# Performance work log

Measured on AMD Instinct MI355X. Metric: run time of the kernel, lower is better.

Reference implementation:

```python
import jax, jax.numpy as jnp
import numpy as np

E = 768
H = 8

def setup_inputs() -> dict:
    key = jax.random.key(0)
    ks = jax.random.split(key, 9)
    s = 1.0 / np.sqrt(E)
    x = jax.random.normal(ks[0], (4, 2048, E), dtype=jnp.float32)
    Wq = jax.random.uniform(ks[1], (E, E), jnp.float32, -s, s)
    bq = jax.random.uniform(ks[2], (E,), jnp.float32, -s, s)
    Wk = jax.random.uniform(ks[3], (E, E), jnp.float32, -s, s)
    bk = jax.random.uniform(ks[4], (E,), jnp.float32, -s, s)
    Wv = jax.random.uniform(ks[5], (E, E), jnp.float32, -s, s)
    bv = jax.random.uniform(ks[6], (E,), jnp.float32, -s, s)
    Wo = jax.random.uniform(ks[7], (E, E), jnp.float32, -s, s)
    bo = jax.random.uniform(ks[8], (E,), jnp.float32, -s, s)
    return {"x": x, "Wq": Wq, "bq": bq, "Wk": Wk, "bk": bk, "Wv": Wv, "bv": bv, "Wo": Wo, "bo": bo}

def reference(x, Wq, bq, Wk, bk, Wv, bv, Wo, bo):
    B, N, Emb = x.shape
    d = Emb // H
    # projections (torch Linear: y = x @ W.T + b)
    q = (x @ Wq.T + bq).reshape(B, N, H, d).transpose(0, 2, 1, 3)  # [B,H,N,d]
    k = (x @ Wk.T + bk).reshape(B, N, H, d).transpose(0, 2, 1, 3)
    v = (x @ Wv.T + bv).reshape(B, N, H, d).transpose(0, 2, 1, 3)
    scores = jnp.einsum('bhnd,bhmd->bhnm', q, k) / jnp.sqrt(jnp.float32(d))
    attn = jax.nn.softmax(scores, axis=-1)  # dropout p=0.0 -> identity
    out = jnp.einsum('bhnm,bhmd->bhnd', attn, v)
    out = out.transpose(0, 2, 1, 3).reshape(B, N, Emb)
    return out @ Wo.T + bo
```

## Files before the change

### kernel.cpp

```cpp
#include <hip/hip_runtime.h>


#define E_DIM 768
#define N_HEAD 8
#define D_HEAD 96
#define B_SZ 4
#define N_SEQ 2048
#define BN (B_SZ * N_SEQ)

typedef unsigned short u16;
typedef __attribute__((ext_vector_type(8))) unsigned short u16x8;
typedef __attribute__((ext_vector_type(4))) unsigned short u16x4;
typedef __attribute__((ext_vector_type(8))) short s16x8;
typedef __attribute__((ext_vector_type(4))) float f32x4;

#define SZ_X   ((size_t)BN * E_DIM)
#define SZ_W   ((size_t)E_DIM * E_DIM)
#define SZ_B   ((size_t)E_DIM)
#define N_CONV (SZ_X + 4 * SZ_W + 4 * SZ_B)

__device__ __forceinline__ float bf2f(u16 u) {
    union { unsigned u; float f; } c; c.u = ((unsigned)u) << 16; return c.f;
}
__device__ __forceinline__ u16 f2bf(float f) {
    union { float f; unsigned u; } c; c.f = f;
    unsigned r = c.u + 0x7FFFu + ((c.u >> 16) & 1u);
    return (u16)(r >> 16);
}
__device__ __forceinline__ void gl_lds16(const u16* g, u16* l) {
    __builtin_amdgcn_global_load_lds(
        (const __attribute__((address_space(1))) unsigned int*)g,
        (__attribute__((address_space(3))) unsigned int*)l, 16, 0, 0);
}

__global__ void detect_dtype(const void* __restrict__ x, int* __restrict__ flag) {
    __shared__ int cnt;
    if (threadIdx.x == 0) cnt = 0;
    __syncthreads();
    const u16* p = (const u16*)x;
    u16 u = p[(size_t)threadIdx.x * 2];
    int ef = (u >> 7) & 0xFF;
    int insane = (ef < 96 || ef > 159) ? 1 : 0;
    atomicAdd(&cnt, insane);
    __syncthreads();
    if (threadIdx.x == 0) *flag = (cnt > 128) ? 1 : 0;
}

__global__ __launch_bounds__(256) void convert_inputs(
    const int* __restrict__ flag,
    const void* __restrict__ x,
    const void* __restrict__ wq, const void* __restrict__ wk,
    const void* __restrict__ wv, const void* __restrict__ wo,
    const void* __restrict__ bq, const void* __restrict__ bk,
    const void* __restrict__ bv, const void* __restrict__ bo,
    u16* __restrict__ dst)
{
    size_t i = (size_t)blockIdx.x * 256 + threadIdx.x;
    if (i >= N_CONV) return;
    const int f32 = *flag;
    size_t r = i;
    const void* s;
    if (r < SZ_X) { s = x; }
    else { r -= SZ_X;
      if (r < SZ_W) { s = wq; }
      else { r -= SZ_W;
        if (r < SZ_W) { s = wk; }
        else { r -= SZ_W;
          if (r < SZ_W) { s = wv; }
          else { r -= SZ_W;
            if (r < SZ_W) { s = wo; }
            else { r -= SZ_W;
              if (r < SZ_B) { s = bq; }
              else { r -= SZ_B;
                if (r < SZ_B) { s = bk; }
                else { r -= SZ_B;
                  if (r < SZ_B) { s = bv; }
                  else { r -= SZ_B; s = bo; }
                }
              }
            }
          }
        }
      }
    }
    dst[i] = f32 ? f2bf(((const float*)s)[r]) : ((const u16*)s)[r];
}

#define GBK 32

__global__ __launch_bounds__(256) void gemm_mfma_qkv(
    const u16* __restrict__ A, const u16* __restrict__ W,
    const u16* __restrict__ bias, u16* __restrict__ C)
{
    __shared__ u16 As[128 * GBK];
    __shared__ u16 Bs[128 * GBK];
    const int tid = threadIdx.x;
    const int wave = tid >> 6, lane = tid & 63;
    const int q4 = lane >> 4, l16 = lane & 15;
    const int wm = wave & 1, wn = wave >> 1;
    const int bm = blockIdx.x, bn = blockIdx.y;
    const int lrow = lane >> 2, lcs = lane & 3;

    f32x4 acc[4][4];
    #pragma unroll
    for (int i = 0; i < 4; i++)
        #pragma unroll
        for (int j = 0; j < 4; j++) acc[i][j] = (f32x4){0.f, 0.f, 0.f, 0.f};

    const u16* Ab = A + (size_t)(bm * 128) * E_DIM;
    const u16* Wb = W + (size_t)(bn * 128) * E_DIM;

    for (int kt = 0; kt < E_DIM; kt += GBK) {
        __syncthreads();
        #pragma unroll
        for (int i = 0; i < 2; i++) {
            int r0 = wave * 32 + i * 16;
            gl_lds16(Ab + (size_t)(r0 + lrow) * E_DIM + kt + lcs * 8, &As[r0 * GBK]);
            gl_lds16(Wb + (size_t)(r0 + lrow) * E_DIM + kt + lcs * 8, &Bs[r0 * GBK]);
        }
        __syncthreads();
        s16x8 af[4], bf[4];
        #pragma unroll
        for (int mi = 0; mi < 4; mi++)
            af[mi] = *(const s16x8*)&As[(wm * 64 + mi * 16 + l16) * GBK + q4 * 8];
        #pragma unroll
        for (int ni = 0; ni < 4; ni++)
            bf[ni] = *(const s16x8*)&Bs[(wn * 64 + ni * 16 + l16) * GBK + q4 * 8];
        #pragma unroll
        for (int mi = 0; mi < 4; mi++)
            #pragma unroll
            for (int ni = 0; ni < 4; ni++)
                acc[mi][ni] = __builtin_amdgcn_mfma_f32_16x16x32_bf16(af[mi], bf[ni], acc[mi][ni], 0, 0, 0);
    }

    #pragma unroll
    for (int ni = 0; ni < 4; ni++) {
        int n = bn * 128 + wn * 64 + ni * 16 + l16;
        int which = n / 768;
        int nc = n - which * 768;
        float bi = bf2f(bias[n]);
        u16* Cw = C + ((size_t)which * BN) * E_DIM;
        #pragma unroll
        for (int mi = 0; mi < 4; mi++) {
            int m = bm * 128 + wm * 64 + mi * 16 + q4 * 4;
            #pragma unroll
            for (int r = 0; r < 4; r++)
                Cw[(size_t)(m + r) * E_DIM + nc] = f2bf(acc[mi][ni][r] + bi);
        }
    }
}

__global__ __launch_bounds__(256) void gemm_mfma_out(
    const u16* __restrict__ A, const u16* __restrict__ W,
    const u16* __restrict__ bias, void* __restrict__ C,
    const int* __restrict__ flag)
{
    __shared__ u16 As[128 * GBK];
    __shared__ u16 Bs[128 * GBK];
    const int tid = threadIdx.x;
    const int wave = tid >> 6, lane = tid & 63;
    const int q4 = lane >> 4, l16 = lane & 15;
    const int wm = wave & 1, wn = wave >> 1;
    const int bm = blockIdx.x, bn = blockIdx.y;
    const int lrow = lane >> 2, lcs = lane & 3;

    f32x4 acc[4][4];
    #pragma unroll
    for (int i = 0; i < 4; i++)
        #pragma unroll
        for (int j = 0; j < 4; j++) acc[i][j] = (f32x4){0.f, 0.f, 0.f, 0.f};

    const u16* Ab = A + (size_t)(bm * 128) * E_DIM;
    const u16* Wb = W + (size_t)(bn * 128) * E_DIM;

    for (int kt = 0; kt < E_DIM; kt += GBK) {
        __syncthreads();
        #pragma unroll
        for (int i = 0; i < 2; i++) {
            int r0 = wave * 32 + i * 16;
            gl_lds16(Ab + (size_t)(r0 + lrow) * E_DIM + kt + lcs * 8, &As[r0 * GBK]);
            gl_lds16(Wb + (size_t)(r0 + lrow) * E_DIM + kt + lcs * 8, &Bs[r0 * GBK]);
        }
        __syncthreads();
        s16x8 af[4], bf[4];
        #pragma unroll
        for (int mi = 0; mi < 4; mi++)
            af[mi] = *(const s16x8*)&As[(wm * 64 + mi * 16 + l16) * GBK + q4 * 8];
        #pragma unroll
        for (int ni = 0; ni < 4; ni++)
            bf[ni] = *(const s16x8*)&Bs[(wn * 64 + ni * 16 + l16) * GBK + q4 * 8];
        #pragma unroll
        for (int mi = 0; mi < 4; mi++)
            #pragma unroll
            for (int ni = 0; ni < 4; ni++)
                acc[mi][ni] = __builtin_amdgcn_mfma_f32_16x16x32_bf16(af[mi], bf[ni], acc[mi][ni], 0, 0, 0);
    }

    const int f32 = *flag;
    #pragma unroll
    for (int ni = 0; ni < 4; ni++) {
        int n = bn * 128 + wn * 64 + ni * 16 + l16;
        float bi = bf2f(bias[n]);
        #pragma unroll
        for (int mi = 0; mi < 4; mi++) {
            int m = bm * 128 + wm * 64 + mi * 16 + q4 * 4;
            #pragma unroll
            for (int r = 0; r < 4; r++) {
                float v = acc[mi][ni][r] + bi;
                if (f32) ((float*)C)[(size_t)(m + r) * E_DIM + n] = v;
                else     ((u16*)C)[(size_t)(m + r) * E_DIM + n] = f2bf(v);
            }
        }
    }
}

__global__ __launch_bounds__(256) void transpose_v(
    const u16* __restrict__ V, u16* __restrict__ Vt)
{
    __shared__ u16 t[32][33];
    const int bh = blockIdx.z, b = bh >> 3, h = bh & 7;
    const int n0 = blockIdx.x * 32, d0 = blockIdx.y * 32;
    const int tx = threadIdx.x & 31, ty = threadIdx.x >> 5;
    #pragma unroll
    for (int i = 0; i < 4; i++) {
        int r = ty + i * 8;
        t[r][tx] = V[(size_t)(b * N_SEQ + n0 + r) * E_DIM + h * D_HEAD + d0 + tx];
    }
    __syncthreads();
    #pragma unroll
    for (int i = 0; i < 4; i++) {
        int r = ty + i * 8;
        Vt[(size_t)((b * N_HEAD + h) * D_HEAD + d0 + r) * N_SEQ + n0 + tx] = t[tx][r];
    }
}

#define QT2 128
#define KT 64

__global__ __launch_bounds__(512) void attn_mfma2(
    const u16* __restrict__ Q, const u16* __restrict__ K,
    const u16* __restrict__ Vt, u16* __restrict__ O)
{
    __shared__ u16 Ks[3 * 64 * 32];
    __shared__ u16 Vts[2 * 96 * 32];
    __shared__ u16 Ps[8 * 16 * 72];

    const int tid = threadIdx.x;
    const int wave = tid >> 6, lane = tid & 63;
    const int q4 = lane >> 4, l16 = lane & 15;
    const int swz = (l16 >> 1) & 3;
    const int b = blockIdx.z, h = blockIdx.y, qb = blockIdx.x;

    const float SCL2 = 0.10206207261596577f * 1.4426950408889634f;

    const int qrow = qb * QT2 + wave * 16 + l16;
    const u16* qptr = Q + (size_t)(b * N_SEQ + qrow) * E_DIM + h * D_HEAD;
    s16x8 qf[3];
    #pragma unroll
    for (int ks = 0; ks < 3; ks++) {
        u16x8 raw = *(const u16x8*)(qptr + ks * 32 + q4 * 8);
        #pragma unroll
        for (int j = 0; j < 8; j++)
            qf[ks][j] = (short)f2bf(bf2f(raw[j]) * SCL2);
    }

    f32x4 of[6];
    #pragma unroll
    for (int i = 0; i < 6; i++) of[i] = (f32x4){0.f, 0.f, 0.f, 0.f};
    float l_r[4] = {0.f, 0.f, 0.f, 0.f};

    u16* psw = Ps + wave * 16 * 72;

    for (int kt = 0; kt < N_SEQ; kt += KT) {
        __syncthreads();
        #pragma unroll
        for (int ii = 0; ii < 3; ii++) {
            int t = wave + 8 * ii;
            if (t < 12) {
                int plane = t >> 2, sub = t & 3;
                int cip = sub * 64 + lane;
                int r = cip >> 2;
                int cs2 = (cip & 3) ^ ((r >> 1) & 3);
                gl_lds16(K + (size_t)(b * N_SEQ + kt + r) * E_DIM + h * D_HEAD + plane * 32 + cs2 * 8,
                         &Ks[plane * 2048 + sub * 512]);
            } else {
                int j = t - 12;
                int plane = j / 6, sub = j - plane * 6;
                int cip = sub * 64 + lane;
                int r = cip >> 2;
                int cs2 = (cip & 3) ^ ((r >> 1) & 3);
                gl_lds16(Vt + (size_t)((b * N_HEAD + h) * D_HEAD + r) * N_SEQ + kt + plane * 32 + cs2 * 8,
                         &Vts[plane * 3072 + sub * 512]);
            }
        }
        __syncthreads();

        f32x4 sf[4];
        #pragma unroll
        for (int i = 0; i < 4; i++) sf[i] = (f32x4){0.f, 0.f, 0.f, 0.f};
        #pragma unroll
        for (int nt = 0; nt < 4; nt++)
            #pragma unroll
            for (int ks = 0; ks < 3; ks++) {
                s16x8 bfr = *(const s16x8*)&Ks[ks * 2048 + (nt * 16 + l16) * 32 + ((q4 ^ swz) << 3)];
                sf[nt] = __builtin_amdgcn_mfma_f32_16x16x32_bf16(qf[ks], bfr, sf[nt], 0, 0, 0);
            }

        #pragma unroll
        for (int nt = 0; nt < 4; nt++)
            #pragma unroll
            for (int r = 0; r < 4; r++) {
                float pv = exp2f(sf[nt][r]);
                l_r[r] += pv;
                psw[(q4 * 4 + r) * 72 + nt * 16 + l16] = f2bf(pv);
            }

        #pragma unroll
        for (int ks2 = 0; ks2 < 2; ks2++) {
            s16x8 afr = *(const s16x8*)&psw[l16 * 72 + ks2 * 32 + q4 * 8];
            #pragma unroll
            for (int nt = 0; nt < 6; nt++) {
                s16x8 bfr = *(const s16x8*)&Vts[ks2 * 3072 + (nt * 16 + l16) * 32 + ((q4 ^ swz) << 3)];
                of[nt] = __builtin_amdgcn_mfma_f32_16x16x32_bf16(afr, bfr, of[nt], 0, 0, 0);
            }
        }
    }

    float linv[4];
    #pragma unroll
    for (int r = 0; r < 4; r++) {
        float l = l_r[r];
        #pragma unroll
        for (int off = 1; off < 16; off <<= 1)
            l += __shfl_xor(l, off, 64);
        linv[r] = 1.0f / l;
    }
    u16* optr = O + (size_t)(b * N_SEQ + qb * QT2 + wave * 16) * E_DIM + h * D_HEAD;
    #pragma unroll
    for (int nt = 0; nt < 6; nt++)
        #pragma unroll
        for (int r = 0; r < 4; r++)
            optr[(size_t)(q4 * 4 + r) * E_DIM + nt * 16 + l16] = f2bf(of[nt][r] * linv[r]);
}

extern "C" void kernel_launch(void* const* d_in, const int* in_sizes, int n_in,
                              void* d_out, int out_size, void* d_ws, size_t ws_size,
                              hipStream_t stream) {
    (void)in_sizes; (void)n_in; (void)out_size; (void)ws_size;
    const void* x  = d_in[0];
    const void* Wq = d_in[1]; const void* bq = d_in[2];
    const void* Wk = d_in[3]; const void* bk = d_in[4];
    const void* Wv = d_in[5]; const void* bv = d_in[6];
    const void* Wo = d_in[7]; const void* bo = d_in[8];

    int* flag = (int*)d_ws;
    u16* base = (u16*)d_ws + 8;
    u16* xb  = base;
    u16* wqb = xb  + SZ_X;
    u16* wob = wqb + 3 * SZ_W;
    u16* bqb = wob + SZ_W;
    u16* bob = bqb + 3 * SZ_B;
    u16* q_ws = bob + SZ_B;
    u16* k_ws = q_ws + SZ_X;
    u16* v_ws = k_ws + SZ_X;
    u16* vt_ws = v_ws + SZ_X;
    u16* o_ws = v_ws;

    detect_dtype<<<1, 256, 0, stream>>>(x, flag);
    convert_inputs<<<(int)((N_CONV + 255) / 256), 256, 0, stream>>>(
        flag, x, Wq, Wk, Wv, Wo, bq, bk, bv, bo, base);

    gemm_mfma_qkv<<<dim3(BN / 128, 2304 / 128), 256, 0, stream>>>(xb, wqb, bqb, q_ws);

    transpose_v<<<dim3(N_SEQ / 32, D_HEAD / 32, B_SZ * N_HEAD), 256, 0, stream>>>(
        v_ws, vt_ws);

    attn_mfma2<<<dim3(N_SEQ / QT2, N_HEAD, B_SZ), 512, 0, stream>>>(
        q_ws, k_ws, vt_ws, o_ws);

    gemm_mfma_out<<<dim3(BN / 128, E_DIM / 128), 256, 0, stream>>>(
        o_ws, wob, bob, d_out, flag);
}
```

Baseline: 295.0 us.

## Fuse V transpose into projection GEMM, vectorize conversion and epilogue stores

```diff
diff --git a/kernel.cpp b/kernel.cpp
--- a/kernel.cpp
+++ b/kernel.cpp
@@ -46,7 +46,7 @@
     if (threadIdx.x == 0) *flag = (cnt > 128) ? 1 : 0;
 }
 
-__global__ __launch_bounds__(256) void convert_inputs(
+__global__ __launch_bounds__(256) void convert8(
     const int* __restrict__ flag,
     const void* __restrict__ x,
     const void* __restrict__ wq, const void* __restrict__ wk,
@@ -55,7 +55,7 @@
     const void* __restrict__ bv, const void* __restrict__ bo,
     u16* __restrict__ dst)
 {
-    size_t i = (size_t)blockIdx.x * 256 + threadIdx.x;
+    size_t i = ((size_t)blockIdx.x * 256 + threadIdx.x) * 8;
     if (i >= N_CONV) return;
     const int f32 = *flag;
     size_t r = i;
@@ -83,17 +83,52 @@
         }
       }
     }
-    dst[i] = f32 ? f2bf(((const float*)s)[r]) : ((const u16*)s)[r];
+    u16x8 o;
+    if (f32) {
+        float4 a = ((const float4*)((const float*)s + r))[0];
+        float4 b = ((const float4*)((const float*)s + r))[1];
+        o[0] = f2bf(a.x); o[1] = f2bf(a.y); o[2] = f2bf(a.z); o[3] = f2bf(a.w);
+        o[4] = f2bf(b.x); o[5] = f2bf(b.y); o[6] = f2bf(b.z); o[7] = f2bf(b.w);
+    } else {
+        o = *(const u16x8*)((const u16*)s + r);
+    }
+    *(u16x8*)(dst + i) = o;
 }
 
 #define GBK 32
 
-__global__ __launch_bounds__(256) void gemm_mfma_qkv(
+#define GEMM_KLOOP(Ab, Wb)                                                            \
+    for (int kt = 0; kt < E_DIM; kt += GBK) {                                         \
+        __syncthreads();                                                              \
+        _Pragma("unroll")                                                             \
+        for (int i = 0; i < 2; i++) {                                                 \
+            int r0 = wave * 32 + i * 16;                                              \
+            gl_lds16(Ab + (size_t)(r0 + lrow) * E_DIM + kt + lcs * 8, &As[r0 * GBK]); \
+            gl_lds16(Wb + (size_t)(r0 + lrow) * E_DIM + kt + lcs * 8, &Bs[r0 * GBK]); \
+        }                                                                             \
+        __syncthreads();                                                              \
+        s16x8 af[4], bf[4];                                                           \
+        _Pragma("unroll")                                                             \
+        for (int mi = 0; mi < 4; mi++)                                                \
+            af[mi] = *(const s16x8*)&As[(wm * 64 + mi * 16 + l16) * GBK + q4 * 8];    \
+        _Pragma("unroll")                                                             \
+        for (int ni = 0; ni < 4; ni++)                                                \
+            bf[ni] = *(const s16x8*)&Bs[(wn * 64 + ni * 16 + l16) * GBK + q4 * 8];    \
+        _Pragma("unroll")                                                             \
+        for (int mi = 0; mi < 4; mi++)                                                \
+            _Pragma("unroll")                                                         \
+            for (int ni = 0; ni < 4; ni++)                                            \
+                acc[mi][ni] = __builtin_amdgcn_mfma_f32_16x16x32_bf16(                \
+                    af[mi], bf[ni], acc[mi][ni], 0, 0, 0);                            \
+    }
+
+__global__ __launch_bounds__(256) void gemm_mfma_qk(
     const u16* __restrict__ A, const u16* __restrict__ W,
     const u16* __restrict__ bias, u16* __restrict__ C)
 {
     __shared__ u16 As[128 * GBK];
     __shared__ u16 Bs[128 * GBK];
+    __shared__ u16 Cb[32 * 136];
     const int tid = threadIdx.x;
     const int wave = tid >> 6, lane = tid & 63;
     const int q4 = lane >> 4, l16 = lane & 15;
@@ -109,44 +144,71 @@
 
     const u16* Ab = A + (size_t)(bm * 128) * E_DIM;
     const u16* Wb = W + (size_t)(bn * 128) * E_DIM;
-
-    for (int kt = 0; kt < E_DIM; kt += GBK) {
-        __syncthreads();
-        #pragma unroll
-        for (int i = 0; i < 2; i++) {
-            int r0 = wave * 32 + i * 16;
-            gl_lds16(Ab + (size_t)(r0 + lrow) * E_DIM + kt + lcs * 8, &As[r0 * GBK]);
-            gl_lds16(Wb + (size_t)(r0 + lrow) * E_DIM + kt + lcs * 8, &Bs[r0 * GBK]);
-        }
-        __syncthreads();
-        s16x8 af[4], bf[4];
-        #pragma unroll
-        for (int mi = 0; mi < 4; mi++)
-            af[mi] = *(const s16x8*)&As[(wm * 64 + mi * 16 + l16) * GBK + q4 * 8];
-        #pragma unroll
-        for (int ni = 0; ni < 4; ni++)
-            bf[ni] = *(const s16x8*)&Bs[(wn * 64 + ni * 16 + l16) * GBK + q4 * 8];
-        #pragma unroll
-        for (int mi = 0; mi < 4; mi++)
-            #pragma unroll
-            for (int ni = 0; ni < 4; ni++)
-                acc[mi][ni] = __builtin_amdgcn_mfma_f32_16x16x32_bf16(af[mi], bf[ni], acc[mi][ni], 0, 0, 0);
-    }
-
-    #pragma unroll
-    for (int ni = 0; ni < 4; ni++) {
-        int n = bn * 128 + wn * 64 + ni * 16 + l16;
-        int which = n / 768;
-        int nc = n - which * 768;
-        float bi = bf2f(bias[n]);
-        u16* Cw = C + ((size_t)which * BN) * E_DIM;
-        #pragma unroll
-        for (int mi = 0; mi < 4; mi++) {
-            int m = bm * 128 + wm * 64 + mi * 16 + q4 * 4;
+    GEMM_KLOOP(Ab, Wb)
+
+    u16* Cw = C + (size_t)(bn / 6) * SZ_X;
+    const int nc0 = (bn % 6) * 128;
+    const int row = tid >> 3, seg = (tid & 7) * 16;
+    #pragma unroll
+    for (int mi = 0; mi < 4; mi++) {
+        __syncthreads();
+        #pragma unroll
+        for (int ni = 0; ni < 4; ni++) {
+            int n_l = wn * 64 + ni * 16 + l16;
+            float bi = bf2f(bias[bn * 128 + n_l]);
             #pragma unroll
             for (int r = 0; r < 4; r++)
-                Cw[(size_t)(m + r) * E_DIM + nc] = f2bf(acc[mi][ni][r] + bi);
-        }
+                Cb[(wm * 16 + q4 * 4 + r) * 136 + n_l] = f2bf(acc[mi][ni][r] + bi);
+        }
+        __syncthreads();
+        int mrow = bm * 128 + (row >> 4) * 64 + mi * 16 + (row & 15);
+        *(u16x8*)(Cw + (size_t)mrow * E_DIM + nc0 + seg)     = *(const u16x8*)&Cb[row * 136 + seg];
+        *(u16x8*)(Cw + (size_t)mrow * E_DIM + nc0 + seg + 8) = *(const u16x8*)&Cb[row * 136 + seg + 8];
+    }
+}
+
+__global__ __launch_bounds__(256) void gemm_mfma_v(
+    const u16* __restrict__ A, const u16* __restrict__ W,
+    const u16* __restrict__ bias, u16* __restrict__ Vt)
+{
+    __shared__ u16 As[128 * GBK];
+    __shared__ u16 Bs[128 * GBK];
+    __shared__ u16 Cb[128 * 40];
+    const int tid = threadIdx.x;
+    const int wave = tid >> 6, lane = tid & 63;
+    const int q4 = lane >> 4, l16 = lane & 15;
+    const int wm = wave & 1, wn = wave >> 1;
+    const int bm = blockIdx.x, bn = blockIdx.y;
+    const int lrow = lane >> 2, lcs = lane & 3;
+
+    f32x4 acc[4][4];
+    #pragma unroll
+    for (int i = 0; i < 4; i++)
+        #pragma unroll
+        for (int j = 0; j < 4; j++) acc[i][j] = (f32x4){0.f, 0.f, 0.f, 0.f};
+
+    const u16* Ab = A + (size_t)(bm * 128) * E_DIM;
+    const u16* Wb = W + (size_t)(bn * 128) * E_DIM;
+    GEMM_KLOOP(Ab, Wb)
+
+    const int b = bm >> 4;
+    const int n_l = tid >> 1, m0 = (tid & 1) * 16;
+    const size_t vrow = (size_t)(b * 768 + bn * 128 + n_l);
+    #pragma unroll
+    for (int mi = 0; mi < 4; mi++) {
+        __syncthreads();
+        #pragma unroll
+        for (int ni = 0; ni < 4; ni++) {
+            int nl = wn * 64 + ni * 16 + l16;
+            float bi = bf2f(bias[bn * 128 + nl]);
+            #pragma unroll
+            for (int r = 0; r < 4; r++)
+                Cb[nl * 40 + wm * 16 + q4 * 4 + r] = f2bf(acc[mi][ni][r] + bi);
+        }
+        __syncthreads();
+        int seq0 = (bm & 15) * 128 + (tid & 1) * 64 + mi * 16;
+        *(u16x8*)(Vt + vrow * N_SEQ + seq0)     = *(const u16x8*)&Cb[n_l * 40 + m0];
+        *(u16x8*)(Vt + vrow * N_SEQ + seq0 + 8) = *(const u16x8*)&Cb[n_l * 40 + m0 + 8];
     }
 }
 
@@ -157,6 +219,7 @@
 {
     __shared__ u16 As[128 * GBK];
     __shared__ u16 Bs[128 * GBK];
+    __shared__ float Cbf[32 * 132];
     const int tid = threadIdx.x;
     const int wave = tid >> 6, lane = tid & 63;
     const int q4 = lane >> 4, l16 = lane & 15;
@@ -172,65 +235,38 @@
 
     const u16* Ab = A + (size_t)(bm * 128) * E_DIM;
     const u16* Wb = W + (size_t)(bn * 128) * E_DIM;
-
-    for (int kt = 0; kt < E_DIM; kt += GBK) {
-        __syncthreads();
-        #pragma unroll
-        for (int i = 0; i < 2; i++) {
-            int r0 = wave * 32 + i * 16;
-            gl_lds16(Ab + (size_t)(r0 + lrow) * E_DIM + kt + lcs * 8, &As[r0 * GBK]);
-            gl_lds16(Wb + (size_t)(r0 + lrow) * E_DIM + kt + lcs * 8, &Bs[r0 * GBK]);
-        }
-        __syncthreads();
-        s16x8 af[4], bf[4];
-        #pragma unroll
-        for (int mi = 0; mi < 4; mi++)
-            af[mi] = *(const s16x8*)&As[(wm * 64 + mi * 16 + l16) * GBK + q4 * 8];
-        #pragma unroll
-        for (int ni = 0; ni < 4; ni++)
-            bf[ni] = *(const s16x8*)&Bs[(wn * 64 + ni * 16 + l16) * GBK + q4 * 8];
-        #pragma unroll
-        for (int mi = 0; mi < 4; mi++)
-            #pragma unroll
-            for (int ni = 0; ni < 4; ni++)
-                acc[mi][ni] = __builtin_amdgcn_mfma_f32_16x16x32_bf16(af[mi], bf[ni], acc[mi][ni], 0, 0, 0);
-    }
+    GEMM_KLOOP(Ab, Wb)
 
     const int f32 = *flag;
-    #pragma unroll
-    for (int ni = 0; ni < 4; ni++) {
-        int n = bn * 128 + wn * 64 + ni * 16 + l16;
-        float bi = bf2f(bias[n]);
-        #pragma unroll
-        for (int mi = 0; mi < 4; mi++) {
-            int m = bm * 128 + wm * 64 + mi * 16 + q4 * 4;
-            #pragma unroll
-            for (int r = 0; r < 4; r++) {
-                float v = acc[mi][ni][r] + bi;
-                if (f32) ((float*)C)[(size_t)(m + r) * E_DIM + n] = v;
-                else     ((u16*)C)[(size_t)(m + r) * E_DIM + n] = f2bf(v);
-            }
-        }
-    }
-}
-
-__global__ __launch_bounds__(256) void transpose_v(
-    const u16* __restrict__ V, u16* __restrict__ Vt)
-{
-    __shared__ u16 t[32][33];
-    const int bh = blockIdx.z, b = bh >> 3, h = bh & 7;
-    const int n0 = blockIdx.x * 32, d0 = blockIdx.y * 32;
-    const int tx = threadIdx.x & 31, ty = threadIdx.x >> 5;
-    #pragma unroll
-    for (int i = 0; i < 4; i++) {
-        int r = ty + i * 8;
-        t[r][tx] = V[(size_t)(b * N_SEQ + n0 + r) * E_DIM + h * D_HEAD + d0 + tx];
-    }
-    __syncthreads();
-    #pragma unroll
-    for (int i = 0; i < 4; i++) {
-        int r = ty + i * 8;
-        Vt[(size_t)((b * N_HEAD + h) * D_HEAD + d0 + r) * N_SEQ + n0 + tx] = t[tx][r];
+    const int row = tid >> 3, seg = (tid & 7) * 16;
+    #pragma unroll
+    for (int mi = 0; mi < 4; mi++) {
+        __syncthreads();
+        #pragma unroll
+        for (int ni = 0; ni < 4; ni++) {
+            int n_l = wn * 64 + ni * 16 + l16;
+            float bi = bf2f(bias[bn * 128 + n_l]);
+            #pragma unroll
+            for (int r = 0; r < 4; r++)
+                Cbf[(wm * 16 + q4 * 4 + r) * 132 + n_l] = acc[mi][ni][r] + bi;
+        }
+        __syncthreads();
+        int mrow = bm * 128 + (row >> 4) * 64 + mi * 16 + (row & 15);
+        if (f32) {
+            #pragma unroll
+            for (int c = 0; c < 4; c++)
+                *(float4*)((float*)C + (size_t)mrow * E_DIM + bn * 128 + seg + c * 4) =
+                    *(const float4*)&Cbf[row * 132 + seg + c * 4];
+        } else {
+            u16x8 o0, o1;
+            #pragma unroll
+            for (int c = 0; c < 8; c++) {
+                o0[c] = f2bf(Cbf[row * 132 + seg + c]);
+                o1[c] = f2bf(Cbf[row * 132 + seg + 8 + c]);
+            }
+            *(u16x8*)((u16*)C + (size_t)mrow * E_DIM + bn * 128 + seg)     = o0;
+            *(u16x8*)((u16*)C + (size_t)mrow * E_DIM + bn * 128 + seg + 8) = o1;
+        }
     }
 }
 
@@ -357,23 +393,22 @@
     u16* base = (u16*)d_ws + 8;
     u16* xb  = base;
     u16* wqb = xb  + SZ_X;
+    u16* wvb = wqb + 2 * SZ_W;
     u16* wob = wqb + 3 * SZ_W;
     u16* bqb = wob + SZ_W;
+    u16* bvb = bqb + 2 * SZ_B;
     u16* bob = bqb + 3 * SZ_B;
     u16* q_ws = bob + SZ_B;
     u16* k_ws = q_ws + SZ_X;
-    u16* v_ws = k_ws + SZ_X;
-    u16* vt_ws = v_ws + SZ_X;
-    u16* o_ws = v_ws;
+    u16* vt_ws = k_ws + SZ_X;
+    u16* o_ws = vt_ws + SZ_X;
 
     detect_dtype<<<1, 256, 0, stream>>>(x, flag);
-    convert_inputs<<<(int)((N_CONV + 255) / 256), 256, 0, stream>>>(
+    convert8<<<(int)((N_CONV / 8 + 255) / 256), 256, 0, stream>>>(
         flag, x, Wq, Wk, Wv, Wo, bq, bk, bv, bo, base);
 
-    gemm_mfma_qkv<<<dim3(BN / 128, 2304 / 128), 256, 0, stream>>>(xb, wqb, bqb, q_ws);
-
-    transpose_v<<<dim3(N_SEQ / 32, D_HEAD / 32, B_SZ * N_HEAD), 256, 0, stream>>>(
-        v_ws, vt_ws);
+    gemm_mfma_qk<<<dim3(BN / 128, 1536 / 128), 256, 0, stream>>>(xb, wqb, bqb, q_ws);
+    gemm_mfma_v <<<dim3(BN / 128,  768 / 128), 256, 0, stream>>>(xb, wvb, bvb, vt_ws);
 
     attn_mfma2<<<dim3(N_SEQ / QT2, N_HEAD, B_SZ), 512, 0, stream>>>(
         q_ws, k_ws, vt_ws, o_ws);
```

New measurement: 281.0 us. 4.7% less time.
